# Optimization experiments

Measured on AMD Instinct MI355X. Metric: run time of the kernel, lower is better.

The kernel has to match this reference:

```python
import jax, jax.numpy as jnp
import numpy as np
from jax import lax

V, E, H = 128, 32, 128  # vocab, embed_dim, hidden_size
B, S = 4, 512


def setup_inputs() -> dict:
    key = jax.random.key(0)
    ks = jax.random.split(key, 14)
    sc = 0.05
    return {
        "x": jax.random.randint(ks[0], (B, S), 0, V),
        "emb": jax.random.normal(ks[1], (V, E), jnp.float32) * sc,
        "W_ih": jax.random.normal(ks[2], (4 * H, E), jnp.float32) * sc,
        "W_hh": jax.random.normal(ks[3], (4 * H, H), jnp.float32) * sc,
        "b_ih": jax.random.normal(ks[4], (4 * H,), jnp.float32) * sc,
        "b_hh": jax.random.normal(ks[5], (4 * H,), jnp.float32) * sc,
        "Wq": jax.random.normal(ks[6], (H, H), jnp.float32) * sc,
        "bq": jax.random.normal(ks[7], (H,), jnp.float32) * sc,
        "Wk": jax.random.normal(ks[8], (H, H), jnp.float32) * sc,
        "bk": jax.random.normal(ks[9], (H,), jnp.float32) * sc,
        "v": jax.random.normal(ks[10], (H,), jnp.float32) * sc,
        "Wf": jax.random.normal(ks[11], (V, 2 * H), jnp.float32) * sc,
        "bf": jax.random.normal(ks[12], (V,), jnp.float32) * sc,
    }


def _lstm(e, W_ih, W_hh, b_ih, b_hh):
    # e: (B, S, E) -> outputs (B, S, H); PyTorch gate order i, f, g, o
    b, s, _ = e.shape
    h0 = jnp.zeros((b, H), e.dtype)
    c0 = jnp.zeros((b, H), e.dtype)
    bias = b_ih + b_hh

    def step(carry, xt):
        h, c = carry
        g = xt @ W_ih.T + h @ W_hh.T + bias  # (B, 4H)
        i, f, gg, o = jnp.split(g, 4, axis=-1)
        c = jax.nn.sigmoid(f) * c + jax.nn.sigmoid(i) * jnp.tanh(gg)
        h = jax.nn.sigmoid(o) * jnp.tanh(c)
        return (h, c), h

    (hT, cT), hs = lax.scan(step, (h0, c0), jnp.swapaxes(e, 0, 1))
    return jnp.swapaxes(hs, 0, 1), hT, cT


def reference(x, emb, W_ih, W_hh, b_ih, b_hh, Wq, bq, Wk, bk, v, Wf, bf):
    e = emb[x]  # (B, S, E)
    out, hT, cT = _lstm(e, W_ih, W_hh, b_ih, b_hh)  # (B, S, H)
    s = out.shape[1]
    q = out @ Wq.T + bq  # (B, S, H)
    k = out @ Wk.T + bk  # (B, S, H)
    # Bahdanau additive scores: v^T tanh(q_t + k_i) -> (B, S, S)
    t = jnp.tanh(q[:, :, None, :] + k[:, None, :, :])  # (B, S, S, H)
    scores = jnp.einsum('bsth,h->bst', t, v)
    mask = jnp.tril(jnp.ones((s, s), bool))
    scores = jnp.where(mask[None], scores, -jnp.inf)
    w = jax.nn.softmax(scores, axis=-1)
    ctx = jnp.einsum('bst,bth->bsh', w, out)
    logits = jnp.concatenate([out, ctx], axis=-1) @ Wf.T + bf  # (B, S, V)
    return logits, hT, cT
```

## Files before the change

kernel.cpp:

```cpp
#include <hip/hip_runtime.h>

#define Vn 128
#define En 32
#define Hn 128
#define Bn 4
#define Sn 512
#define G4H 512

typedef _Float16 half8 __attribute__((ext_vector_type(8)));
typedef float    floatx4 __attribute__((ext_vector_type(4)));

__device__ __forceinline__ float frcp(float x) {
    return __builtin_amdgcn_rcpf(x);
}

__device__ __forceinline__ float fsigmoid(float x) {
    return frcp(1.0f + __expf(-x));
}

__device__ __forceinline__ float ftanh(float x) {
    float e = __expf(2.0f * x);
    return 1.0f - 2.0f * frcp(e + 1.0f);
}

__global__ __attribute__((amdgpu_flat_work_group_size(512, 512),
                          amdgpu_waves_per_eu(2, 2)))
void k_lstm(
        const float* __restrict__ emb, const float* __restrict__ Wih,
        const float* __restrict__ bih, const float* __restrict__ bhh,
        const float* __restrict__ Whh, float* __restrict__ Gtab,
        const int* __restrict__ x,
        float* __restrict__ out, float* __restrict__ hT, float* __restrict__ cT) {
    int tid = threadIdx.x;
    int wv  = tid >> 6;
    int l   = tid & 63;
    int cn  = l & 15;
    int kg  = l >> 4;
    int cb  = l & 3;
    int jr  = l >> 2;
    int bb  = l & 3;
    int aj  = 16 * wv + jr;

    bool r1 = (l >> 2) & 1;
    bool r2 = (l >> 2) & 2;

    __shared__ float elds[Vn][En];
    __shared__ int xb[4][520];
    __shared__ alignas(16) _Float16 hbuf[2][4][144];

    for (int i = tid; i < Vn * En; i += 512) ((float*)elds)[i] = emb[i];
    for (int i = tid; i < Bn * Sn; i += 512) xb[i >> 9][i & 511] = x[i] * 2048;
    if (tid < 4) xb[tid][512] = 0;
    for (int i = tid; i < 2 * 4 * 144; i += 512) ((_Float16*)hbuf)[i] = (_Float16)0.0f;
    __syncthreads();

    {
        int jg = tid;
        const float4* wr = (const float4*)(Wih + jg * En);
        float4 w[8];
#pragma unroll
        for (int i = 0; i < 8; i++) w[i] = wr[i];
        float bias = bih[jg] + bhh[jg];
        int dst = (jg & 127) * 4 + (jg >> 7);
        for (int v = 0; v < Vn; v++) {
            const float4* e4 = (const float4*)elds[v];
            float acc = bias;
#pragma unroll
            for (int i = 0; i < 8; i++) {
                float4 e = e4[i];
                acc += w[i].x * e.x + w[i].y * e.y + w[i].z * e.z + w[i].w * e.w;
            }
            Gtab[v * G4H + dst] = acc;
        }
    }

    half8 af[4][4];
#pragma unroll
    for (int g = 0; g < 4; g++) {
#pragma unroll
        for (int kc = 0; kc < 4; kc++) {
            int row = g * Hn + 16 * wv + cn;
            int kb  = kc * 32 + kg * 8;
            const float4* p = (const float4*)(Whh + row * Hn + kb);
            float4 lo = p[0], hi = p[1];
            half8 a = { (_Float16)lo.x, (_Float16)lo.y, (_Float16)lo.z, (_Float16)lo.w,
                        (_Float16)hi.x, (_Float16)hi.y, (_Float16)hi.z, (_Float16)hi.w };
            af[g][kc] = a;
        }
    }

    float c_ = 0.f, h_ = 0.f;
    const char* gbase = (const char*)Gtab + aj * 16;
    float* outp = out + bb * Sn * Hn + aj;
    __syncthreads();

    float4 gx4 = *(const float4*)(gbase + xb[bb][0]);

#pragma unroll 2
    for (int s = 0; s < Sn; s++) {
        half8 bf[4];
#pragma unroll
        for (int kc = 0; kc < 4; kc++)
            bf[kc] = *(const half8*)&hbuf[s & 1][cb][kc * 32 + kg * 8];

        floatx4 d[4];
#pragma unroll
        for (int g = 0; g < 4; g++) {
            floatx4 acc = { 0.f, 0.f, 0.f, 0.f };
#pragma unroll
            for (int kc = 0; kc < 4; kc++)
                acc = __builtin_amdgcn_mfma_f32_16x16x32_f16(af[g][kc], bf[kc], acc, 0, 0, 0);
            d[g] = acc;
        }

        float4 ngx = *(const float4*)(gbase + xb[bb][s + 1]);

        float ex[4];
#pragma unroll
        for (int g = 0; g < 4; g++) {
            float lo = r1 ? d[g][1] : d[g][0];
            float hi = r1 ? d[g][3] : d[g][2];
            ex[g] = r2 ? hi : lo;
        }

        float gi = gx4.x + ex[0];
        float gf = gx4.y + ex[1];
        float gg = gx4.z + ex[2];
        float go = gx4.w + ex[3];
        c_ = fsigmoid(gf) * c_ + fsigmoid(gi) * ftanh(gg);
        h_ = fsigmoid(go) * ftanh(c_);

        *outp = h_;  outp += Hn;
        hbuf[(s & 1) ^ 1][bb][aj] = (_Float16)h_;

        gx4 = ngx;
        asm volatile("s_waitcnt lgkmcnt(0)\n\ts_barrier" ::: "memory");
    }
    hT[bb * Hn + aj] = h_;
    cT[bb * Hn + aj] = c_;
}

__global__ __launch_bounds__(128) void k_k(
        const float* __restrict__ out, const float* __restrict__ Wk,
        const float* __restrict__ bk, float* __restrict__ koT) {
    int bs  = blockIdx.x;
    int b   = bs >> 9;
    int s   = bs & (Sn - 1);
    int tid = threadIdx.x;
    __shared__ float o[Hn];
    o[tid] = out[bs * Hn + tid];
    __syncthreads();
    const float4* wr = (const float4*)(Wk + tid * Hn);
    float acc = bk[tid];
#pragma unroll
    for (int i = 0; i < Hn / 4; i++) {
        float4 w4 = wr[i];
        acc += w4.x * o[4*i] + w4.y * o[4*i+1] + w4.z * o[4*i+2] + w4.w * o[4*i+3];
    }
    koT[b * 65536 + (tid >> 2) * 2048 + s * 4 + (tid & 3)] = acc;
}

__global__ __launch_bounds__(512) void k_attn(
        const float* __restrict__ koT, const float* __restrict__ vvec,
        const float* __restrict__ out,
        const float* __restrict__ Wq, const float* __restrict__ bq,
        const float* __restrict__ Wf, const float* __restrict__ bf,
        float* __restrict__ logits) {
    int b   = blockIdx.x >> 9;
    int t   = blockIdx.x & (Sn - 1);
    int tid = threadIdx.x;
    int wv  = tid >> 6;
    __shared__ float qs[Hn];
    __shared__ float vs[Hn];
    __shared__ float oc[2 * Hn];
    __shared__ float sc[Sn];
    __shared__ float wmax[8];
    __shared__ float wsum[8];
    __shared__ float part[16][Hn];

    if (tid < Hn) {
        oc[tid] = out[(b * Sn + t) * Hn + tid];
        vs[tid] = vvec[tid];
    }
    __syncthreads();

    {
        int h = tid & 127, kq = tid >> 7;
        const float4* wr = (const float4*)(Wq + h * Hn + kq * 32);
        const float* ob = oc + kq * 32;
        float a = 0.0f;
#pragma unroll
        for (int i = 0; i < 8; i++) {
            float4 w4 = wr[i];
            a += w4.x * ob[4*i] + w4.y * ob[4*i+1] + w4.z * ob[4*i+2] + w4.w * ob[4*i+3];
        }
        part[kq][h] = a;
    }
    __syncthreads();
    if (tid < Hn)
        qs[tid] = bq[tid] + part[0][tid] + part[1][tid] + part[2][tid] + part[3][tid];
    __syncthreads();

    float a = -1e30f;
    if (tid <= t) {
        const float4* kT = (const float4*)koT + b * 16384 + tid;
        float s = 0.0f;
#pragma unroll
        for (int u = 0; u < Hn / 4; u++) {
            float4 k4 = kT[u * 512];
            s += vs[4*u]   * ftanh(qs[4*u]   + k4.x);
            s += vs[4*u+1] * ftanh(qs[4*u+1] + k4.y);
            s += vs[4*u+2] * ftanh(qs[4*u+2] + k4.z);
            s += vs[4*u+3] * ftanh(qs[4*u+3] + k4.w);
        }
        sc[tid] = s;
        a = s;
    }
#pragma unroll
    for (int off = 32; off > 0; off >>= 1) a = fmaxf(a, __shfl_xor(a, off));
    if ((tid & 63) == 0) wmax[wv] = a;
    __syncthreads();
    float m = wmax[0];
#pragma unroll
    for (int r = 1; r < 8; r++) m = fmaxf(m, wmax[r]);

    float ev = 0.0f;
    if (tid <= t) {
        ev = __expf(sc[tid] - m);
        sc[tid] = ev;
    }
    float ssum = ev;
#pragma unroll
    for (int off = 32; off > 0; off >>= 1) ssum += __shfl_xor(ssum, off);
    if ((tid & 63) == 0) wsum[wv] = ssum;
    __syncthreads();
    float tot = wsum[0];
#pragma unroll
    for (int r = 1; r < 8; r++) tot += wsum[r];
    float inv = frcp(tot);

    int hq = tid & 31;
    int is = tid >> 5;
    float4 acc = {0.0f, 0.0f, 0.0f, 0.0f};
    const float4* ob4 = (const float4*)(out + b * Sn * Hn);
    for (int i = is; i <= t; i += 16) {
        float s = sc[i];
        float4 o4 = ob4[i * (Hn / 4) + hq];
        acc.x += s * o4.x; acc.y += s * o4.y;
        acc.z += s * o4.z; acc.w += s * o4.w;
    }
    ((float4*)part[is])[hq] = acc;
    __syncthreads();
    if (tid < Hn) {
        float sum2 = 0.0f;
#pragma unroll
        for (int r = 0; r < 16; r++) sum2 += part[r][tid];
        oc[Hn + tid] = sum2 * inv;
    }
    __syncthreads();

    {
        int v = tid & 127, kq = tid >> 7;
        const float4* wr = (const float4*)(Wf + v * 2 * Hn + kq * 64);
        const float* ob = oc + kq * 64;
        float a2 = 0.0f;
#pragma unroll
        for (int i = 0; i < 16; i++) {
            float4 w4 = wr[i];
            a2 += w4.x * ob[4*i] + w4.y * ob[4*i+1] + w4.z * ob[4*i+2] + w4.w * ob[4*i+3];
        }
        part[kq][v] = a2;
    }
    __syncthreads();
    if (tid < Hn)
        logits[(b * Sn + t) * Vn + tid] =
            bf[tid] + part[0][tid] + part[1][tid] + part[2][tid] + part[3][tid];
}

extern "C" void kernel_launch(void* const* d_in, const int* in_sizes, int n_in,
                              void* d_out, int out_size, void* d_ws, size_t ws_size,
                              hipStream_t stream) {
    const int*   x   = (const int*)d_in[0];
    const float* emb = (const float*)d_in[1];
    const float* Wih = (const float*)d_in[2];
    const float* Whh = (const float*)d_in[3];
    const float* bih = (const float*)d_in[4];
    const float* bhh = (const float*)d_in[5];
    const float* Wq  = (const float*)d_in[6];
    const float* bq  = (const float*)d_in[7];
    const float* Wk  = (const float*)d_in[8];
    const float* bk  = (const float*)d_in[9];
    const float* v   = (const float*)d_in[10];
    const float* Wf  = (const float*)d_in[11];
    const float* bf  = (const float*)d_in[12];

    float* logits = (float*)d_out;
    float* hT     = logits + Bn * Sn * Vn;
    float* cT     = hT + Bn * Hn;

    float* ws   = (float*)d_ws;
    float* Gtab = ws;
    float* outb = ws + 65536;
    float* koT  = ws + 65536 + 262144;

    k_lstm<<<1, 512, 0, stream>>>(emb, Wih, bih, bhh, Whh, Gtab, x, outb, hT, cT);
    k_k<<<Bn * Sn, 128, 0, stream>>>(outb, Wk, bk, koT);
    k_attn<<<Bn * Sn, 512, 0, stream>>>(koT, v, outb, Wq, bq, Wf, bf, logits);
}
```

Measured before the change: 442.5 us.

## Prescale gate inputs by log2e and seed MFMA accumulators with input projections

Result: slower. 649.4 us (+46.8%).

```diff
diff --git a/kernel.cpp b/kernel.cpp
--- a/kernel.cpp
+++ b/kernel.cpp
@@ -7,6 +7,9 @@
 #define Sn 512
 #define G4H 512
 
+#define L2E  1.4426950408889634f
+#define T2E  2.8853900817779268f
+
 typedef _Float16 half8 __attribute__((ext_vector_type(8)));
 typedef float    floatx4 __attribute__((ext_vector_type(4)));
 
@@ -14,13 +17,17 @@
     return __builtin_amdgcn_rcpf(x);
 }
 
-__device__ __forceinline__ float fsigmoid(float x) {
-    return frcp(1.0f + __expf(-x));
-}
-
-__device__ __forceinline__ float ftanh(float x) {
-    float e = __expf(2.0f * x);
-    return 1.0f - 2.0f * frcp(e + 1.0f);
+#if __has_builtin(__builtin_amdgcn_exp2f)
+__device__ __forceinline__ float fexp2(float x) { return __builtin_amdgcn_exp2f(x); }
+#else
+__device__ __forceinline__ float fexp2(float x) { return __expf(x * 0.69314718056f); }
+#endif
+
+__device__ __forceinline__ float fsig2(float x) {
+    return frcp(1.0f + fexp2(-x));
+}
+__device__ __forceinline__ float ftan2(float x) {
+    return 1.0f - 2.0f * frcp(fexp2(x) + 1.0f);
 }
 
 __global__ __attribute__((amdgpu_flat_work_group_size(512, 512),
@@ -61,7 +68,7 @@
 #pragma unroll
         for (int i = 0; i < 8; i++) w[i] = wr[i];
         float bias = bih[jg] + bhh[jg];
-        int dst = (jg & 127) * 4 + (jg >> 7);
+        float scl  = ((jg >> 7) == 2) ? T2E : L2E;
         for (int v = 0; v < Vn; v++) {
             const float4* e4 = (const float4*)elds[v];
             float acc = bias;
@@ -70,31 +77,40 @@
                 float4 e = e4[i];
                 acc += w[i].x * e.x + w[i].y * e.y + w[i].z * e.z + w[i].w * e.w;
             }
-            Gtab[v * G4H + dst] = acc;
+            Gtab[v * G4H + jg] = acc * scl;
         }
     }
 
     half8 af[4][4];
 #pragma unroll
     for (int g = 0; g < 4; g++) {
+        float scl = (g == 2) ? T2E : L2E;
 #pragma unroll
         for (int kc = 0; kc < 4; kc++) {
             int row = g * Hn + 16 * wv + cn;
             int kb  = kc * 32 + kg * 8;
             const float4* p = (const float4*)(Whh + row * Hn + kb);
             float4 lo = p[0], hi = p[1];
-            half8 a = { (_Float16)lo.x, (_Float16)lo.y, (_Float16)lo.z, (_Float16)lo.w,
-                        (_Float16)hi.x, (_Float16)hi.y, (_Float16)hi.z, (_Float16)hi.w };
+            half8 a = { (_Float16)(lo.x * scl), (_Float16)(lo.y * scl),
+                        (_Float16)(lo.z * scl), (_Float16)(lo.w * scl),
+                        (_Float16)(hi.x * scl), (_Float16)(hi.y * scl),
+                        (_Float16)(hi.z * scl), (_Float16)(hi.w * scl) };
             af[g][kc] = a;
         }
     }
 
     float c_ = 0.f, h_ = 0.f;
-    const char* gbase = (const char*)Gtab + aj * 16;
+    const char* gkb = (const char*)Gtab + wv * 64 + kg * 16;
     float* outp = out + bb * Sn * Hn + aj;
     __syncthreads();
 
-    float4 gx4 = *(const float4*)(gbase + xb[bb][0]);
+    floatx4 gx[4];
+    {
+        int xo = xb[bb][0];
+#pragma unroll
+        for (int g = 0; g < 4; g++)
+            gx[g] = *(const floatx4*)(gkb + xo + g * 512);
+    }
 
 #pragma unroll 2
     for (int s = 0; s < Sn; s++) {
@@ -106,14 +122,19 @@
         floatx4 d[4];
 #pragma unroll
         for (int g = 0; g < 4; g++) {
-            floatx4 acc = { 0.f, 0.f, 0.f, 0.f };
+            floatx4 acc = gx[g];
 #pragma unroll
             for (int kc = 0; kc < 4; kc++)
                 acc = __builtin_amdgcn_mfma_f32_16x16x32_f16(af[g][kc], bf[kc], acc, 0, 0, 0);
             d[g] = acc;
         }
 
-        float4 ngx = *(const float4*)(gbase + xb[bb][s + 1]);
+        {
+            int xo = xb[bb][s + 1];
+#pragma unroll
+            for (int g = 0; g < 4; g++)
+                gx[g] = *(const floatx4*)(gkb + xo + g * 512);
+        }
 
         float ex[4];
 #pragma unroll
@@ -123,17 +144,12 @@
             ex[g] = r2 ? hi : lo;
         }
 
-        float gi = gx4.x + ex[0];
-        float gf = gx4.y + ex[1];
-        float gg = gx4.z + ex[2];
-        float go = gx4.w + ex[3];
-        c_ = fsigmoid(gf) * c_ + fsigmoid(gi) * ftanh(gg);
-        h_ = fsigmoid(go) * ftanh(c_);
+        c_ = fsig2(ex[1]) * c_ + fsig2(ex[0]) * ftan2(ex[2]);
+        h_ = fsig2(ex[3]) * ftan2(c_ * T2E);
 
         *outp = h_;  outp += Hn;
         hbuf[(s & 1) ^ 1][bb][aj] = (_Float16)h_;
 
-        gx4 = ngx;
         asm volatile("s_waitcnt lgkmcnt(0)\n\ts_barrier" ::: "memory");
     }
     hT[bb * Hn + aj] = h_;
@@ -157,7 +173,7 @@
         float4 w4 = wr[i];
         acc += w4.x * o[4*i] + w4.y * o[4*i+1] + w4.z * o[4*i+2] + w4.w * o[4*i+3];
     }
-    koT[b * 65536 + (tid >> 2) * 2048 + s * 4 + (tid & 3)] = acc;
+    koT[b * 65536 + (tid >> 2) * 2048 + s * 4 + (tid & 3)] = acc * T2E;
 }
 
 __global__ __launch_bounds__(512) void k_attn(
@@ -198,7 +214,7 @@
     }
     __syncthreads();
     if (tid < Hn)
-        qs[tid] = bq[tid] + part[0][tid] + part[1][tid] + part[2][tid] + part[3][tid];
+        qs[tid] = T2E * (bq[tid] + part[0][tid] + part[1][tid] + part[2][tid] + part[3][tid]);
     __syncthreads();
 
     float a = -1e30f;
@@ -208,10 +224,10 @@
 #pragma unroll
         for (int u = 0; u < Hn / 4; u++) {
             float4 k4 = kT[u * 512];
-            s += vs[4*u]   * ftanh(qs[4*u]   + k4.x);
-            s += vs[4*u+1] * ftanh(qs[4*u+1] + k4.y);
-            s += vs[4*u+2] * ftanh(qs[4*u+2] + k4.z);
-            s += vs[4*u+3] * ftanh(qs[4*u+3] + k4.w);
+            s += vs[4*u]   * ftan2(qs[4*u]   + k4.x);
+            s += vs[4*u+1] * ftan2(qs[4*u+1] + k4.y);
+            s += vs[4*u+2] * ftan2(qs[4*u+2] + k4.z);
+            s += vs[4*u+3] * ftan2(qs[4*u+3] + k4.w);
         }
         sc[tid] = s;
         a = s;
```
